# Kernel optimization log

Measured on AMD Instinct MI355X. Metric: run time of the kernel, lower is better.

## Reference

```python
import jax, jax.numpy as jnp
import numpy as np

B, U, W = 64, 128, 128  # batch, input_units, window_size (output units == U)

def setup_inputs() -> dict:
    key = jax.random.key(0)
    k1, k2, k3 = jax.random.split(key, 3)
    return {
        "input_tensor": jax.random.normal(k1, (B, U), dtype=jnp.float32),
        "state": jax.random.normal(k2, (B, U, W), dtype=jnp.float32),
        "w": jax.random.normal(k3, (2 * U + 1, U), dtype=jnp.float32) * 0.05,
        "b": jnp.zeros((U,), dtype=jnp.float32),
    }

def reference(input_tensor, state, w, b):
    b_, u_, w_ = state.shape
    # state @ state_shift is exactly a left-shift along the window axis
    new_state = jnp.concatenate([state[:, :, 1:], input_tensor[:, :, None]], axis=-1)  # [B,U,W]
    # NOTE: original uses tf.reshape (NOT transpose) [B,U,W] -> [B,W,U]; we replicate that
    flip = new_state.reshape(b_, w_, u_)                      # [B,W,U]
    # h_i[b,i,j,:] = flip[b,j,:] (stacked on axis=1); h_j[b,i,j,:] = flip[b,i,:]
    dot = jnp.einsum('biu,bju->bij', flip, flip)              # h_i . h_j, [B,W,W]
    w_hi, w_hj, w_dot = w[:u_], w[u_:2 * u_], w[2 * u_]       # split concat-matmul
    sim = (jnp.einsum('bju,uv->bjv', flip, w_hi)[:, None, :, :]   # h_i part
           + jnp.einsum('biu,uv->biv', flip, w_hj)[:, :, None, :] # h_j part
           + dot[..., None] * w_dot + b)                          # [B,W,W,U]
    a = jax.nn.softmax(sim, axis=2)                           # softmax over axis=-2 (j)
    c = jnp.einsum('bju,biju->biu', flip, a)                  # sum_j h_i * a_ij
    return c[:, -1, :]                                        # c_last, [B,U]
```

## Files before the change

### kernel.cpp

```cpp
#include <hip/hip_runtime.h>
#include <hip/hip_bf16.h>

constexpr int Bx = 64, Ux = 128, Wx = 128;
constexpr int NS = 4;
constexpr int VC = Ux / NS;
constexpr int LDF = 129;
constexpr int LDA = 129;

__global__ __launch_bounds__(256) void rsa_kernel(const float* __restrict__ input,
                                                  const float* __restrict__ state,
                                                  const float* __restrict__ w,
                                                  float* __restrict__ out) {
  __shared__ float flip_s[Wx][LDF];
  __shared__ float a_s[VC][LDA];
  __shared__ __align__(16) float ws[Ux][VC];
  __shared__ __align__(16) float wdot_s[VC];
  __shared__ float dot_s[Wx];
  __shared__ float dotp[2][Wx];
  __shared__ float red_s[8][VC];

  const int t = threadIdx.x;
  const int s = blockIdx.x;
  const int b = blockIdx.y;
  const int vbase = s * VC;

  const float* stb = state + (size_t)b * Ux * Wx;
  const float* inb = input + (size_t)b * Ux;

  for (int idx = t; idx < Wx * Ux; idx += 256) {
    int j = idx >> 7, u = idx & 127;
    flip_s[j][u] = (u < Wx - 1) ? stb[j * Wx + u + 1] : inb[j];
  }
  for (int idx = t; idx < Ux * VC; idx += 256) {
    int u = idx >> 5, v = idx & (VC - 1);
    ws[u][v] = w[u * Ux + vbase + v];
  }
  if (t < VC) wdot_s[t] = w[2 * Ux * Ux + vbase + t];
  __syncthreads();

  {
    int j = t & 127, h = t >> 7;
    int u0 = h * 64;
    float p = 0.f;
#pragma unroll
    for (int u = 0; u < 64; ++u)
      p = fmaf(flip_s[j][u0 + u], flip_s[Wx - 1][u0 + u], p);
    dotp[h][j] = p;
  }
  __syncthreads();
  if (t < Wx) dot_s[t] = dotp[0][t] + dotp[1][t];
  __syncthreads();

  const int vgrp = t & 7;
  const int jg = t >> 3;
  const int j0 = jg * 4;
  float acc[4][4];
#pragma unroll
  for (int a0 = 0; a0 < 4; ++a0)
#pragma unroll
    for (int a1 = 0; a1 < 4; ++a1) acc[a0][a1] = 0.f;

#pragma unroll 4
  for (int u = 0; u < Ux; ++u) {
    float4 wv = *reinterpret_cast<const float4*>(&ws[u][vgrp * 4]);
#pragma unroll
    for (int jj = 0; jj < 4; ++jj) {
      float f = flip_s[j0 + jj][u];
      acc[jj][0] = fmaf(f, wv.x, acc[jj][0]);
      acc[jj][1] = fmaf(f, wv.y, acc[jj][1]);
      acc[jj][2] = fmaf(f, wv.z, acc[jj][2]);
      acc[jj][3] = fmaf(f, wv.w, acc[jj][3]);
    }
  }
  {
    float4 wd = *reinterpret_cast<const float4*>(&wdot_s[vgrp * 4]);
#pragma unroll
    for (int jj = 0; jj < 4; ++jj) {
      float dj = dot_s[j0 + jj];
      a_s[vgrp * 4 + 0][j0 + jj] = fmaf(dj, wd.x, acc[jj][0]);
      a_s[vgrp * 4 + 1][j0 + jj] = fmaf(dj, wd.y, acc[jj][1]);
      a_s[vgrp * 4 + 2][j0 + jj] = fmaf(dj, wd.z, acc[jj][2]);
      a_s[vgrp * 4 + 3][j0 + jj] = fmaf(dj, wd.w, acc[jj][3]);
    }
  }
  __syncthreads();

  const int v = t & 31, sub = t >> 5;
  const int jb = sub * 16;
  float m = -3.4e38f;
#pragma unroll
  for (int k = 0; k < 16; ++k) m = fmaxf(m, a_s[v][jb + k]);
  red_s[sub][v] = m;
  __syncthreads();
  float M = red_s[0][v];
#pragma unroll
  for (int r = 1; r < 8; ++r) M = fmaxf(M, red_s[r][v]);
  __syncthreads();

  float ssum = 0.f;
#pragma unroll
  for (int k = 0; k < 16; ++k) {
    float e = __expf(a_s[v][jb + k] - M);
    a_s[v][jb + k] = e;
    ssum += e;
  }
  red_s[sub][v] = ssum;
  __syncthreads();
  float S = 0.f;
#pragma unroll
  for (int r = 0; r < 8; ++r) S += red_s[r][v];
  __syncthreads();

  float p = 0.f;
#pragma unroll
  for (int k = 0; k < 16; ++k) {
    int j = jb + k;
    p = fmaf(flip_s[j][vbase + v], a_s[v][j], p);
  }
  red_s[sub][v] = p;
  __syncthreads();
  if (sub == 0) {
    float o = 0.f;
#pragma unroll
    for (int r = 0; r < 8; ++r) o += red_s[r][v];
    out[(size_t)b * Ux + vbase + v] = o / S;
  }
}

extern "C" void kernel_launch(void* const* d_in, const int* in_sizes, int n_in,
                              void* d_out, int out_size, void* d_ws, size_t ws_size,
                              hipStream_t stream) {
  const float* input = (const float*)d_in[0];
  const float* state = (const float*)d_in[1];
  const float* w     = (const float*)d_in[2];
  float* out = (float*)d_out;
  dim3 grid(NS, Bx);
  rsa_kernel<<<grid, dim3(256), 0, stream>>>(input, state, w, out);
}
```

Before: 74.60 us.

## Use bf16 MFMA for projection and dot products with shifted-window correction

Converts the state tile and the weight slice to bf16 in shared memory. The projection and the dot products against the last row are computed with 16x16x32 bf16 MFMA instructions instead of scalar fp32 FMAs. The unshifted state is staged with vectorized float4 loads, and the window shift is handled by index offsets plus a rank-one correction term. This is meant to remove the scalar FMA cost and the strided gather. In exchange it lowers precision to bf16 and adds correction logic that must be exactly right.

```diff
diff --git a/kernel.cpp b/kernel.cpp
--- a/kernel.cpp
+++ b/kernel.cpp
@@ -3,84 +3,106 @@
 
 constexpr int Bx = 64, Ux = 128, Wx = 128;
 constexpr int NS = 4;
-constexpr int VC = Ux / NS;
-constexpr int LDF = 129;
-constexpr int LDA = 129;
+constexpr int VC = 32;
+constexpr int LDST = 136;
+constexpr int LDWT = 136;
+constexpr int LDA  = 129;
+
+typedef __attribute__((ext_vector_type(8))) short s16x8;
+typedef __attribute__((ext_vector_type(4))) float fx4;
+
+static __device__ __forceinline__ short f2b(float x) {
+  union { float f; unsigned u; } c; c.f = x;
+  unsigned r = c.u + 0x7fffu + ((c.u >> 16) & 1u);
+  return (short)(r >> 16);
+}
+static __device__ __forceinline__ float b2f(short s) {
+  union { unsigned u; float f; } c; c.u = ((unsigned)(unsigned short)s) << 16;
+  return c.f;
+}
 
 __global__ __launch_bounds__(256) void rsa_kernel(const float* __restrict__ input,
                                                   const float* __restrict__ state,
                                                   const float* __restrict__ w,
                                                   float* __restrict__ out) {
-  __shared__ float flip_s[Wx][LDF];
+  __shared__ __align__(16) short st_s[Wx][LDST];
+  __shared__ __align__(16) short wst[VC][LDWT];
   __shared__ float a_s[VC][LDA];
-  __shared__ __align__(16) float ws[Ux][VC];
-  __shared__ __align__(16) float wdot_s[VC];
-  __shared__ float dot_s[Wx];
-  __shared__ float dotp[2][Wx];
   __shared__ float red_s[8][VC];
+  __shared__ float wdot_s[VC], w127_s[VC];
+  __shared__ float dpart[4];
 
   const int t = threadIdx.x;
-  const int s = blockIdx.x;
-  const int b = blockIdx.y;
-  const int vbase = s * VC;
-
+  const int s = blockIdx.x, b = blockIdx.y;
+  const int vb = s * VC;
   const float* stb = state + (size_t)b * Ux * Wx;
   const float* inb = input + (size_t)b * Ux;
 
-  for (int idx = t; idx < Wx * Ux; idx += 256) {
-    int j = idx >> 7, u = idx & 127;
-    flip_s[j][u] = (u < Wx - 1) ? stb[j * Wx + u + 1] : inb[j];
+#pragma unroll
+  for (int i = 0; i < 4; ++i) {
+    int g = i * 4096 + t * 16;
+    int j = g >> 7, k = g & 127;
+    const float4* src = reinterpret_cast<const float4*>(stb + g);
+    float4 x0 = src[0], x1 = src[1], x2 = src[2], x3 = src[3];
+    s16x8 p0 = { f2b(x0.x), f2b(x0.y), f2b(x0.z), f2b(x0.w),
+                 f2b(x1.x), f2b(x1.y), f2b(x1.z), f2b(x1.w) };
+    s16x8 p1 = { f2b(x2.x), f2b(x2.y), f2b(x2.z), f2b(x2.w),
+                 f2b(x3.x), f2b(x3.y), f2b(x3.z), f2b(x3.w) };
+    *reinterpret_cast<s16x8*>(&st_s[j][k])     = p0;
+    *reinterpret_cast<s16x8*>(&st_s[j][k + 8]) = p1;
   }
-  for (int idx = t; idx < Ux * VC; idx += 256) {
-    int u = idx >> 5, v = idx & (VC - 1);
-    ws[u][v] = w[u * Ux + vbase + v];
+  if (t < Wx) st_s[t][128] = f2b(inb[t]);
+  for (int idx = t; idx < 127 * VC; idx += 256) {
+    int r = idx >> 5, v = idx & (VC - 1);
+    wst[v][r + 1] = f2b(w[r * Ux + vb + v]);
   }
-  if (t < VC) wdot_s[t] = w[2 * Ux * Ux + vbase + t];
+  if (t < VC) { wst[t][0] = 0; w127_s[t] = w[127 * Ux + vb + t]; }
+  else if (t < 2 * VC) { wdot_s[t - VC] = w[2 * Ux * Ux + vb + (t - VC)]; }
+  {
+    float part = 0.f;
+    if (t < Wx) { float x = (t < Wx - 1) ? stb[127 * Wx + t + 1] : inb[127]; part = x * x; }
+#pragma unroll
+    for (int off = 32; off; off >>= 1) part += __shfl_down(part, off);
+    if ((t & 63) == 0) dpart[t >> 6] = part;
+  }
   __syncthreads();
 
-  {
-    int j = t & 127, h = t >> 7;
-    int u0 = h * 64;
-    float p = 0.f;
+  const int wv = t >> 6, l = t & 63, lc = l & 15, lg = l >> 4;
+  fx4 accH[2][2] = {};
+  fx4 accD[2]    = {};
 #pragma unroll
-    for (int u = 0; u < 64; ++u)
-      p = fmaf(flip_s[j][u0 + u], flip_s[Wx - 1][u0 + u], p);
-    dotp[h][j] = p;
-  }
-  __syncthreads();
-  if (t < Wx) dot_s[t] = dotp[0][t] + dotp[1][t];
-  __syncthreads();
-
-  const int vgrp = t & 7;
-  const int jg = t >> 3;
-  const int j0 = jg * 4;
-  float acc[4][4];
+  for (int kt = 0; kt < 4; ++kt) {
+    const int ko = kt * 32 + lg * 8;
+    s16x8 bd = *reinterpret_cast<const s16x8*>(&st_s[127][ko]);
+    s16x8 b0 = *reinterpret_cast<const s16x8*>(&wst[lc][ko]);
+    s16x8 b1 = *reinterpret_cast<const s16x8*>(&wst[lc + 16][ko]);
 #pragma unroll
-  for (int a0 = 0; a0 < 4; ++a0)
-#pragma unroll
-    for (int a1 = 0; a1 < 4; ++a1) acc[a0][a1] = 0.f;
-
-#pragma unroll 4
-  for (int u = 0; u < Ux; ++u) {
-    float4 wv = *reinterpret_cast<const float4*>(&ws[u][vgrp * 4]);
-#pragma unroll
-    for (int jj = 0; jj < 4; ++jj) {
-      float f = flip_s[j0 + jj][u];
-      acc[jj][0] = fmaf(f, wv.x, acc[jj][0]);
-      acc[jj][1] = fmaf(f, wv.y, acc[jj][1]);
-      acc[jj][2] = fmaf(f, wv.z, acc[jj][2]);
-      acc[jj][3] = fmaf(f, wv.w, acc[jj][3]);
+    for (int jl = 0; jl < 2; ++jl) {
+      const int jt = wv * 2 + jl;
+      s16x8 a = *reinterpret_cast<const s16x8*>(&st_s[jt * 16 + lc][ko]);
+      accH[jl][0] = __builtin_amdgcn_mfma_f32_16x16x32_bf16(a, b0, accH[jl][0], 0, 0, 0);
+      accH[jl][1] = __builtin_amdgcn_mfma_f32_16x16x32_bf16(a, b1, accH[jl][1], 0, 0, 0);
+      accD[jl]    = __builtin_amdgcn_mfma_f32_16x16x32_bf16(a, bd, accD[jl],    0, 0, 0);
     }
   }
-  {
-    float4 wd = *reinterpret_cast<const float4*>(&wdot_s[vgrp * 4]);
+
+  const float in127  = b2f(st_s[127][128]);
+  const float st0127 = b2f(st_s[127][0]);
+  const float d127   = dpart[0] + dpart[1] + dpart[2] + dpart[3];
+  const float wd0 = wdot_s[lc], wd1 = wdot_s[lc + 16];
+  const float w70 = w127_s[lc], w71 = w127_s[lc + 16];
 #pragma unroll
-    for (int jj = 0; jj < 4; ++jj) {
-      float dj = dot_s[j0 + jj];
-      a_s[vgrp * 4 + 0][j0 + jj] = fmaf(dj, wd.x, acc[jj][0]);
-      a_s[vgrp * 4 + 1][j0 + jj] = fmaf(dj, wd.y, acc[jj][1]);
-      a_s[vgrp * 4 + 2][j0 + jj] = fmaf(dj, wd.z, acc[jj][2]);
-      a_s[vgrp * 4 + 3][j0 + jj] = fmaf(dj, wd.w, acc[jj][3]);
+  for (int jl = 0; jl < 2; ++jl) {
+    const int jt = wv * 2 + jl;
+#pragma unroll
+    for (int r = 0; r < 4; ++r) {
+      const int row = jt * 16 + lg * 4 + r;
+      float st0 = b2f(st_s[row][0]);
+      float inr = b2f(st_s[row][128]);
+      float dotv = accD[jl][r] - st0 * st0127 + inr * in127;
+      if (row == Wx - 1) dotv = d127;
+      a_s[lc][row]      = accH[jl][0][r] + dotv * wd0 + inr * w70;
+      a_s[lc + 16][row] = accH[jl][1][r] + dotv * wd1 + inr * w71;
     }
   }
   __syncthreads();
@@ -96,7 +118,6 @@
 #pragma unroll
   for (int r = 1; r < 8; ++r) M = fmaxf(M, red_s[r][v]);
   __syncthreads();
-
   float ssum = 0.f;
 #pragma unroll
   for (int k = 0; k < 16; ++k) {
@@ -115,7 +136,7 @@
 #pragma unroll
   for (int k = 0; k < 16; ++k) {
     int j = jb + k;
-    p = fmaf(flip_s[j][vbase + v], a_s[v][j], p);
+    p = fmaf(b2f(st_s[j][vb + v + 1]), a_s[v][j], p);
   }
   red_s[sub][v] = p;
   __syncthreads();
@@ -123,7 +144,7 @@
     float o = 0.f;
 #pragma unroll
     for (int r = 0; r < 8; ++r) o += red_s[r][v];
-    out[(size_t)b * Ux + vbase + v] = o / S;
+    out[(size_t)b * Ux + vb + v] = o / S;
   }
 }
 
```

Measured after the change: 66.85 us. 1.12x faster.
